# Kernel optimization log

Hardware: AMD Instinct MI355X
Metric: run time of the kernel (lower is better)

The kernel has to match this reference:

```python
import jax, jax.numpy as jnp
import numpy as np

D_MODEL = 256
N_HEADS = 8
D_K = D_MODEL // N_HEADS
N = 4096
N_SEG = 16


def setup_inputs() -> dict:
    key = jax.random.key(0)
    ks = jax.random.split(key, 12)
    s = 0.02
    x_q = jax.random.normal(ks[0], (N, D_MODEL), jnp.float32)
    x_kv = jax.random.normal(ks[1], (N, D_MODEL), jnp.float32)
    # same key -> identical segment ids so every query segment exists in kv
    batch = jnp.sort(jax.random.randint(ks[2], (N,), 0, N_SEG)).astype(jnp.int64)
    params = {}
    names = ['Wq', 'Wk', 'Wv', 'Wo']
    for i, n in enumerate(names):
        params[n] = jax.random.normal(ks[3 + i], (D_MODEL, D_MODEL), jnp.float32) * s
        params['b' + n[1]] = jnp.zeros((D_MODEL,), jnp.float32)
    return dict(x_q=x_q, x_kv=x_kv, batch_q=batch, batch_kv=batch, **params)


def reference(x_q, x_kv, batch_q, batch_kv, Wq, bq, Wk, bk, Wv, bv, Wo, bo):
    # projections (torch Linear: x @ W.T + b)
    q = (x_q @ Wq.T + bq).reshape(N, N_HEADS, D_K)   # [Nq, H, dk]
    k = (x_kv @ Wk.T + bk).reshape(N, N_HEADS, D_K)  # [Nkv, H, dk]
    v = (x_kv @ Wv.T + bv).reshape(N, N_HEADS, D_K)
    scores = jnp.einsum('qhd,khd->hqk', q, k) / jnp.sqrt(jnp.float32(D_K))
    mask = batch_q[:, None] == batch_kv[None, :]      # block-diagonal [Nq, Nkv]
    scores = jnp.where(mask[None], scores, -jnp.inf)
    attn = jax.nn.softmax(scores, axis=-1)            # [H, Nq, Nkv]
    out = jnp.einsum('hqk,khd->qhd', attn, v).reshape(N, D_MODEL)
    out = out @ Wo.T + bo
    return out, attn[None]  # match torch's [1, H, Nq, Nkv] attn shape
```

## Files before the change

kernel.cpp:

```cpp
#include <hip/hip_runtime.h>

#define N_TOK 4096
#define DM 256
#define NH 8
#define DK 32

using u16 = unsigned short;
using u32 = unsigned int;
using i64 = long long;
typedef float f32x4 __attribute__((ext_vector_type(4)));

__device__ __forceinline__ float bf2f(u16 u){ return __uint_as_float(((u32)u) << 16); }
__device__ __forceinline__ u16 f2bf(float f){
    u32 x = __float_as_uint(f);
    x += 0x7fffu + ((x >> 16) & 1u);
    return (u16)(x >> 16);
}

__global__ __launch_bounds__(256)
void bounds_kernel(const void* __restrict__ batch_q, const void* __restrict__ batch_kv,
                   int2* __restrict__ bounds)
{
    int q = blockIdx.x * 256 + threadIdx.x;
    const int* kv32 = (const int*)batch_kv;
    const i64* kv64 = (const i64*)batch_kv;
    bool is64 = (kv32[N_TOK - 1] == 0);
    int s = is64 ? (int)((const i64*)batch_q)[q] : ((const int*)batch_q)[q];
    int lo = 0, hi = N_TOK;
    while (lo < hi){ int m = (lo + hi) >> 1; int v = is64 ? (int)kv64[m] : kv32[m]; if (v < s) lo = m + 1; else hi = m; }
    int lo2 = lo, hi2 = N_TOK;
    while (lo2 < hi2){ int m = (lo2 + hi2) >> 1; int v = is64 ? (int)kv64[m] : kv32[m]; if (v <= s) lo2 = m + 1; else hi2 = m; }
    bounds[q] = make_int2(lo, lo2);
}

template<int OUT_BF16>
__global__ __launch_bounds__(256)
void proj_kernel(const float* __restrict__ x, const float* __restrict__ W,
                 const float* __restrict__ bias, void* __restrict__ outv)
{
    const int ROWS = 16;
    int row0 = blockIdx.x * ROWS;
    int c = threadIdx.x;
    float acc[ROWS];
    float bv = bias[c];
#pragma unroll
    for (int r = 0; r < ROWS; ++r) acc[r] = bv;
    const float4* Wv = (const float4*)(W + (size_t)c * DM);
    for (int i = 0; i < DM / 4; ++i){
        float4 w = Wv[i];
        int d0 = i * 4;
#pragma unroll
        for (int r = 0; r < ROWS; ++r){
            const float* xr = x + (size_t)(row0 + r) * DM + d0;
            acc[r] += xr[0] * w.x + xr[1] * w.y + xr[2] * w.z + xr[3] * w.w;
        }
    }
#pragma unroll
    for (int r = 0; r < ROWS; ++r){
        size_t idx = (size_t)(row0 + r) * DM + c;
        if (OUT_BF16) ((u16*)outv)[idx] = f2bf(acc[r]);
        else          ((float*)outv)[idx] = acc[r];
    }
}

__global__ __launch_bounds__(256)
void proj_kv_kernel(const float* __restrict__ x, const float* __restrict__ Wk,
                    const float* __restrict__ bk, const float* __restrict__ Wv,
                    const float* __restrict__ bv, u16* __restrict__ Kp,
                    u16* __restrict__ Vp)
{
    const int ROWS = 16;
    int row0 = blockIdx.x * ROWS;
    int c = threadIdx.x;
    int hh = c >> 5, dd = c & 31;
    float acck[ROWS], accv[ROWS];
    float bkv = bk[c], bvv = bv[c];
#pragma unroll
    for (int r = 0; r < ROWS; ++r){ acck[r] = bkv; accv[r] = bvv; }
    const float4* Wk4 = (const float4*)(Wk + (size_t)c * DM);
    const float4* Wv4 = (const float4*)(Wv + (size_t)c * DM);
    for (int i = 0; i < DM / 4; ++i){
        float4 wk = Wk4[i];
        float4 wv = Wv4[i];
        int d0 = i * 4;
#pragma unroll
        for (int r = 0; r < ROWS; ++r){
            const float* xr = x + (size_t)(row0 + r) * DM + d0;
            float x0 = xr[0], x1 = xr[1], x2 = xr[2], x3 = xr[3];
            acck[r] += x0 * wk.x + x1 * wk.y + x2 * wk.z + x3 * wk.w;
            accv[r] += x0 * wv.x + x1 * wv.y + x2 * wv.z + x3 * wv.w;
        }
    }
#pragma unroll
    for (int r = 0; r < ROWS; ++r){
        size_t idx = ((size_t)hh * N_TOK + (row0 + r)) * DK + dd;
        Kp[idx] = f2bf(acck[r]);
        Vp[idx] = f2bf(accv[r]);
    }
}

__global__ __launch_bounds__(256)
void attn_kernel(const float* __restrict__ Q, const u16* __restrict__ K,
                 const u16* __restrict__ V, const int2* __restrict__ bounds,
                 float* __restrict__ attn, float* __restrict__ O)
{
    __shared__ float sc[N_TOK];
    __shared__ float qs[DK];
    __shared__ float red[8];
    __shared__ float Osh[DK];

    int q = blockIdx.x, h = blockIdx.y, tid = threadIdx.x;
    int2 bnd = bounds[q];
    const int lo = bnd.x, hi = bnd.y;
    const u16* Kh = K + (size_t)h * N_TOK * DK;
    const u16* Vh = V + (size_t)h * N_TOK * DK;

    if (tid < DK){ qs[tid] = Q[(size_t)q * DM + h * DK + tid]; Osh[tid] = 0.f; }
    __syncthreads();

    const float scale = 0.17677669529663687f;

    float lmax = -1e30f;
    for (int k = lo + tid; k < hi; k += 256){
        const uint4* kr = (const uint4*)(Kh + (size_t)k * DK);
        float dot = 0.f;
#pragma unroll
        for (int i = 0; i < 4; ++i){
            uint4 p = kr[i];
            dot += qs[i*8+0]*bf2f((u16)p.x) + qs[i*8+1]*bf2f((u16)(p.x>>16));
            dot += qs[i*8+2]*bf2f((u16)p.y) + qs[i*8+3]*bf2f((u16)(p.y>>16));
            dot += qs[i*8+4]*bf2f((u16)p.z) + qs[i*8+5]*bf2f((u16)(p.z>>16));
            dot += qs[i*8+6]*bf2f((u16)p.w) + qs[i*8+7]*bf2f((u16)(p.w>>16));
        }
        dot *= scale;
        sc[k - lo] = dot;
        lmax = fmaxf(lmax, dot);
    }
#pragma unroll
    for (int off = 32; off; off >>= 1) lmax = fmaxf(lmax, __shfl_xor(lmax, off, 64));
    if ((tid & 63) == 0) red[tid >> 6] = lmax;
    __syncthreads();
    float m = fmaxf(fmaxf(red[0], red[1]), fmaxf(red[2], red[3]));

    float lsum = 0.f;
    for (int k = lo + tid; k < hi; k += 256){
        float p = __expf(sc[k - lo] - m);
        sc[k - lo] = p;
        lsum += p;
    }
#pragma unroll
    for (int off = 32; off; off >>= 1) lsum += __shfl_xor(lsum, off, 64);
    if ((tid & 63) == 0) red[4 + (tid >> 6)] = lsum;
    __syncthreads();
    float sum = red[4] + red[5] + red[6] + red[7];
    float inv = (sum > 0.f) ? (1.0f / sum) : 0.f;

    int d2 = tid & 15;
    int g  = tid >> 4;
    float p0 = 0.f, p1 = 0.f;
    for (int k = lo + g; k < hi; k += 16){
        u32 pv = *(const u32*)(Vh + (size_t)k * DK + 2 * d2);
        float p = sc[k - lo];
        p0 += p * bf2f((u16)pv);
        p1 += p * bf2f((u16)(pv >> 16));
    }
    p0 += __shfl_xor(p0, 16, 64); p0 += __shfl_xor(p0, 32, 64);
    p1 += __shfl_xor(p1, 16, 64); p1 += __shfl_xor(p1, 32, 64);
    if ((tid & 63) < 16){
        atomicAdd(&Osh[2 * d2 + 0], p0);
        atomicAdd(&Osh[2 * d2 + 1], p1);
    }

    f32x4* arow4 = (f32x4*)(attn + ((size_t)h * N_TOK + q) * N_TOK);
#pragma unroll
    for (int i = 0; i < N_TOK / 1024; ++i){
        int t = i * 256 + tid;
        int k0 = 4 * t;
        f32x4 w;
        w.x = (k0 + 0 >= lo && k0 + 0 < hi) ? sc[k0 + 0 - lo] * inv : 0.f;
        w.y = (k0 + 1 >= lo && k0 + 1 < hi) ? sc[k0 + 1 - lo] * inv : 0.f;
        w.z = (k0 + 2 >= lo && k0 + 2 < hi) ? sc[k0 + 2 - lo] * inv : 0.f;
        w.w = (k0 + 3 >= lo && k0 + 3 < hi) ? sc[k0 + 3 - lo] * inv : 0.f;
        __builtin_nontemporal_store(w, &arow4[t]);
    }

    __syncthreads();
    if (tid < DK) O[(size_t)q * DM + h * DK + tid] = Osh[tid] * inv;
}

extern "C" void kernel_launch(void* const* d_in, const int* in_sizes, int n_in,
                              void* d_out, int out_size, void* d_ws, size_t ws_size,
                              hipStream_t stream)
{
    const float* x_q  = (const float*)d_in[0];
    const float* x_kv = (const float*)d_in[1];
    const void* batch_q  = d_in[2];
    const void* batch_kv = d_in[3];
    const float* Wq = (const float*)d_in[4];
    const float* bq = (const float*)d_in[5];
    const float* Wk = (const float*)d_in[6];
    const float* bk = (const float*)d_in[7];
    const float* Wv = (const float*)d_in[8];
    const float* bv = (const float*)d_in[9];
    const float* Wo = (const float*)d_in[10];
    const float* bo = (const float*)d_in[11];

    char* ws = (char*)d_ws;
    float* Q  = (float*)ws;
    u16*   Kp = (u16*)(ws + (size_t)4 * 1024 * 1024);
    u16*   Vp = (u16*)(ws + (size_t)6 * 1024 * 1024);
    float* O  = (float*)(ws + (size_t)8 * 1024 * 1024);
    int2* bounds = (int2*)(ws + (size_t)12 * 1024 * 1024);

    float* out  = (float*)d_out;
    float* attn = out + (size_t)N_TOK * DM;

    bounds_kernel<<<N_TOK / 256, 256, 0, stream>>>(batch_q, batch_kv, bounds);
    proj_kernel<0><<<N_TOK/16, 256, 0, stream>>>(x_q,  Wq, bq, Q);
    proj_kv_kernel<<<N_TOK/16, 256, 0, stream>>>(x_kv, Wk, bk, Wv, bv, Kp, Vp);
    attn_kernel<<<dim3(N_TOK, NH), 256, 0, stream>>>(Q, Kp, Vp, bounds, attn, O);
    proj_kernel<0><<<N_TOK/16, 256, 0, stream>>>((const float*)O, Wo, bo, out);
}
```

Baseline: 703.2 us.

## Tile attention over 16 queries with shared K/V chunks and online softmax

```diff
diff --git a/kernel.cpp b/kernel.cpp
--- a/kernel.cpp
+++ b/kernel.cpp
@@ -4,13 +4,16 @@
 #define DM 256
 #define NH 8
 #define DK 32
+#define QT 16
+#define CH 128
 
 using u16 = unsigned short;
 using u32 = unsigned int;
 using i64 = long long;
 typedef float f32x4 __attribute__((ext_vector_type(4)));
 
-__device__ __forceinline__ float bf2f(u16 u){ return __uint_as_float(((u32)u) << 16); }
+__device__ __forceinline__ float bfl(u32 u){ return __uint_as_float(u << 16); }
+__device__ __forceinline__ float bfh(u32 u){ return __uint_as_float(u & 0xffff0000u); }
 __device__ __forceinline__ u16 f2bf(float f){
     u32 x = __float_as_uint(f);
     x += 0x7fffu + ((x >> 16) & 1u);
@@ -100,92 +103,140 @@
 }
 
 __global__ __launch_bounds__(256)
+void zero_kernel(f32x4* __restrict__ p, int n4)
+{
+    int i = blockIdx.x * 256 + threadIdx.x;
+    int stride = gridDim.x * 256;
+    f32x4 z = {0.f, 0.f, 0.f, 0.f};
+    for (; i < n4; i += stride) __builtin_nontemporal_store(z, &p[i]);
+}
+
+__global__ __launch_bounds__(256)
 void attn_kernel(const float* __restrict__ Q, const u16* __restrict__ K,
                  const u16* __restrict__ V, const int2* __restrict__ bounds,
                  float* __restrict__ attn, float* __restrict__ O)
 {
-    __shared__ float sc[N_TOK];
-    __shared__ float qs[DK];
-    __shared__ float red[8];
-    __shared__ float Osh[DK];
-
-    int q = blockIdx.x, h = blockIdx.y, tid = threadIdx.x;
-    int2 bnd = bounds[q];
-    const int lo = bnd.x, hi = bnd.y;
+    __shared__ uint4 kch[CH][5];
+    __shared__ uint4 vch[CH][5];
+
+    const int tid = threadIdx.x;
+    const int ql  = tid >> 4;
+    const int kk  = tid & 15;
+    const int h   = blockIdx.y;
+    const int q0  = blockIdx.x * QT;
+    const int q   = q0 + ql;
+
+    const int2 bq = bounds[q];
+    const int lo = bq.x, hi = bq.y;
+    const int lo_min = bounds[q0].x;
+    const int hi_max = bounds[q0 + QT - 1].y;
+
     const u16* Kh = K + (size_t)h * N_TOK * DK;
     const u16* Vh = V + (size_t)h * N_TOK * DK;
 
-    if (tid < DK){ qs[tid] = Q[(size_t)q * DM + h * DK + tid]; Osh[tid] = 0.f; }
-    __syncthreads();
+    float qr[32];
+    {
+        const float4* qp = (const float4*)(Q + (size_t)q * DM + h * DK);
+#pragma unroll
+        for (int i = 0; i < 8; ++i){
+            float4 t = qp[i];
+            qr[4*i+0] = t.x; qr[4*i+1] = t.y; qr[4*i+2] = t.z; qr[4*i+3] = t.w;
+        }
+    }
 
     const float scale = 0.17677669529663687f;
 
-    float lmax = -1e30f;
-    for (int k = lo + tid; k < hi; k += 256){
-        const uint4* kr = (const uint4*)(Kh + (size_t)k * DK);
-        float dot = 0.f;
-#pragma unroll
-        for (int i = 0; i < 4; ++i){
-            uint4 p = kr[i];
-            dot += qs[i*8+0]*bf2f((u16)p.x) + qs[i*8+1]*bf2f((u16)(p.x>>16));
-            dot += qs[i*8+2]*bf2f((u16)p.y) + qs[i*8+3]*bf2f((u16)(p.y>>16));
-            dot += qs[i*8+4]*bf2f((u16)p.z) + qs[i*8+5]*bf2f((u16)(p.z>>16));
-            dot += qs[i*8+6]*bf2f((u16)p.w) + qs[i*8+7]*bf2f((u16)(p.w>>16));
-        }
-        dot *= scale;
-        sc[k - lo] = dot;
-        lmax = fmaxf(lmax, dot);
-    }
-#pragma unroll
-    for (int off = 32; off; off >>= 1) lmax = fmaxf(lmax, __shfl_xor(lmax, off, 64));
-    if ((tid & 63) == 0) red[tid >> 6] = lmax;
-    __syncthreads();
-    float m = fmaxf(fmaxf(red[0], red[1]), fmaxf(red[2], red[3]));
-
-    float lsum = 0.f;
-    for (int k = lo + tid; k < hi; k += 256){
-        float p = __expf(sc[k - lo] - m);
-        sc[k - lo] = p;
-        lsum += p;
-    }
-#pragma unroll
-    for (int off = 32; off; off >>= 1) lsum += __shfl_xor(lsum, off, 64);
-    if ((tid & 63) == 0) red[4 + (tid >> 6)] = lsum;
-    __syncthreads();
-    float sum = red[4] + red[5] + red[6] + red[7];
-    float inv = (sum > 0.f) ? (1.0f / sum) : 0.f;
-
-    int d2 = tid & 15;
-    int g  = tid >> 4;
-    float p0 = 0.f, p1 = 0.f;
-    for (int k = lo + g; k < hi; k += 16){
-        u32 pv = *(const u32*)(Vh + (size_t)k * DK + 2 * d2);
-        float p = sc[k - lo];
-        p0 += p * bf2f((u16)pv);
-        p1 += p * bf2f((u16)(pv >> 16));
-    }
-    p0 += __shfl_xor(p0, 16, 64); p0 += __shfl_xor(p0, 32, 64);
-    p1 += __shfl_xor(p1, 16, 64); p1 += __shfl_xor(p1, 32, 64);
-    if ((tid & 63) < 16){
-        atomicAdd(&Osh[2 * d2 + 0], p0);
-        atomicAdd(&Osh[2 * d2 + 1], p1);
-    }
-
-    f32x4* arow4 = (f32x4*)(attn + ((size_t)h * N_TOK + q) * N_TOK);
-#pragma unroll
-    for (int i = 0; i < N_TOK / 1024; ++i){
-        int t = i * 256 + tid;
-        int k0 = 4 * t;
-        f32x4 w;
-        w.x = (k0 + 0 >= lo && k0 + 0 < hi) ? sc[k0 + 0 - lo] * inv : 0.f;
-        w.y = (k0 + 1 >= lo && k0 + 1 < hi) ? sc[k0 + 1 - lo] * inv : 0.f;
-        w.z = (k0 + 2 >= lo && k0 + 2 < hi) ? sc[k0 + 2 - lo] * inv : 0.f;
-        w.w = (k0 + 3 >= lo && k0 + 3 < hi) ? sc[k0 + 3 - lo] * inv : 0.f;
-        __builtin_nontemporal_store(w, &arow4[t]);
-    }
-
-    __syncthreads();
-    if (tid < DK) O[(size_t)q * DM + h * DK + tid] = Osh[tid] * inv;
+    float m = -1e30f, s = 0.f;
+    for (int kc = lo_min; kc < hi_max; kc += CH){
+        __syncthreads();
+        for (int e = tid; e < CH * 4; e += 256){
+            int r = e >> 2, p = e & 3;
+            if (kc + r < hi_max)
+                kch[r][p] = *(const uint4*)(Kh + (size_t)(kc + r) * DK + p * 8);
+        }
+        __syncthreads();
+        int kend = min(CH, hi_max - kc);
+        for (int j = kk; j < kend; j += 16){
+            int k = kc + j;
+            if (k < lo || k >= hi) continue;
+            float dot = 0.f;
+#pragma unroll
+            for (int p = 0; p < 4; ++p){
+                uint4 a = kch[j][p];
+                dot += qr[8*p+0]*bfl(a.x) + qr[8*p+1]*bfh(a.x);
+                dot += qr[8*p+2]*bfl(a.y) + qr[8*p+3]*bfh(a.y);
+                dot += qr[8*p+4]*bfl(a.z) + qr[8*p+5]*bfh(a.z);
+                dot += qr[8*p+6]*bfl(a.w) + qr[8*p+7]*bfh(a.w);
+            }
+            float d = dot * scale;
+            float mn = fmaxf(m, d);
+            s = s * __expf(m - mn) + __expf(d - mn);
+            m = mn;
+        }
+    }
+#pragma unroll
+    for (int off = 1; off < 16; off <<= 1){
+        float mo = __shfl_xor(m, off, 64);
+        float so = __shfl_xor(s, off, 64);
+        float mn = fmaxf(m, mo);
+        s = s * __expf(m - mn) + so * __expf(mo - mn);
+        m = mn;
+    }
+    const float inv = (s > 0.f) ? 1.0f / s : 0.f;
+
+    float o[32];
+#pragma unroll
+    for (int d = 0; d < 32; ++d) o[d] = 0.f;
+
+    float* arow = attn + ((size_t)h * N_TOK + q) * N_TOK;
+
+    for (int kc = lo_min; kc < hi_max; kc += CH){
+        __syncthreads();
+        for (int e = tid; e < CH * 4; e += 256){
+            int r = e >> 2, p = e & 3;
+            if (kc + r < hi_max){
+                kch[r][p] = *(const uint4*)(Kh + (size_t)(kc + r) * DK + p * 8);
+                vch[r][p] = *(const uint4*)(Vh + (size_t)(kc + r) * DK + p * 8);
+            }
+        }
+        __syncthreads();
+        int kend = min(CH, hi_max - kc);
+        for (int j = kk; j < kend; j += 16){
+            int k = kc + j;
+            if (k < lo || k >= hi) continue;
+            float dot = 0.f;
+#pragma unroll
+            for (int p = 0; p < 4; ++p){
+                uint4 a = kch[j][p];
+                dot += qr[8*p+0]*bfl(a.x) + qr[8*p+1]*bfh(a.x);
+                dot += qr[8*p+2]*bfl(a.y) + qr[8*p+3]*bfh(a.y);
+                dot += qr[8*p+4]*bfl(a.z) + qr[8*p+5]*bfh(a.z);
+                dot += qr[8*p+6]*bfl(a.w) + qr[8*p+7]*bfh(a.w);
+            }
+            float pr = __expf(dot * scale - m) * inv;
+            __builtin_nontemporal_store(pr, &arow[k]);
+#pragma unroll
+            for (int pp = 0; pp < 4; ++pp){
+                uint4 a = vch[j][pp];
+                o[8*pp+0] += pr * bfl(a.x); o[8*pp+1] += pr * bfh(a.x);
+                o[8*pp+2] += pr * bfl(a.y); o[8*pp+3] += pr * bfh(a.y);
+                o[8*pp+4] += pr * bfl(a.z); o[8*pp+5] += pr * bfh(a.z);
+                o[8*pp+6] += pr * bfl(a.w); o[8*pp+7] += pr * bfh(a.w);
+            }
+        }
+    }
+
+#pragma unroll
+    for (int d = 0; d < 32; ++d){
+#pragma unroll
+        for (int off = 1; off < 16; off <<= 1)
+            o[d] += __shfl_xor(o[d], off, 64);
+    }
+    float s0 = 0.f, s1 = 0.f;
+#pragma unroll
+    for (int d = 0; d < 16; ++d)
+        if (kk == d){ s0 = o[2*d]; s1 = o[2*d + 1]; }
+    *(float2*)(O + (size_t)q * DM + h * DK + 2 * kk) = make_float2(s0, s1);
 }
 
 extern "C" void kernel_launch(void* const* d_in, const int* in_sizes, int n_in,
@@ -215,9 +266,12 @@
     float* out  = (float*)d_out;
     float* attn = out + (size_t)N_TOK * DM;
 
+    int n4 = (int)((size_t)NH * N_TOK * N_TOK / 4);
+    zero_kernel<<<2048, 256, 0, stream>>>((f32x4*)attn, n4);
+
     bounds_kernel<<<N_TOK / 256, 256, 0, stream>>>(batch_q, batch_kv, bounds);
     proj_kernel<0><<<N_TOK/16, 256, 0, stream>>>(x_q,  Wq, bq, Q);
     proj_kv_kernel<<<N_TOK/16, 256, 0, stream>>>(x_kv, Wk, bk, Wv, bv, Kp, Vp);
-    attn_kernel<<<dim3(N_TOK, NH), 256, 0, stream>>>(Q, Kp, Vp, bounds, attn, O);
+    attn_kernel<<<dim3(N_TOK / QT, NH), 256, 0, stream>>>(Q, Kp, Vp, bounds, attn, O);
     proj_kernel<0><<<N_TOK/16, 256, 0, stream>>>((const float*)O, Wo, bo, out);
 }
```

New measurement: 778.3 us. 1.11x slower.
